# Performance work log

Measured on AMD Instinct MI355X. Metric: run time of the kernel, lower is better.

## Reference

```python
import jax, jax.numpy as jnp
import numpy as np

P, Q, R = 6, 0, 0
N = P + Q + R
DIM = 1 << N  # 64 basis blades


def _cayley_table(p, q, r):
    """Dense [dim, dim, dim] Cayley tensor C with C[a, b, a^b] = sign(a, b).
    Basis blades are indexed by bitmasks; sign combines the canonical
    reordering parity with the metric signature (+1 x p, -1 x q, 0 x r)."""
    n = p + q + r
    dim = 1 << n
    metric = [1.0] * p + [-1.0] * q + [0.0] * r
    C = np.zeros((dim, dim, dim), dtype=np.float32)
    for a in range(dim):
        for b in range(dim):
            # reorder parity: count transpositions to sort blade product
            s = 1.0
            aa = a >> 1
            cnt = 0
            while aa:
                cnt += bin(aa & b).count('1')
                aa >>= 1
            if cnt & 1:
                s = -s
            # metric contribution from repeated basis vectors
            for i in range(n):
                if (a >> i) & 1 and (b >> i) & 1:
                    s *= metric[i]
            C[a, b, a ^ b] = s
    return C

CAYLEY = jnp.asarray(_cayley_table(P, Q, R))  # [64, 64, 64], highly sparse


def setup_inputs() -> dict:
    key = jax.random.key(0)
    kx, kw = jax.random.split(key)
    x = jax.random.normal(kx, (1048576, DIM), dtype=jnp.float32)
    weight = jax.random.normal(kw, (DIM,), dtype=jnp.float32)
    return {"x": x, "weight": weight}


def reference(x, weight):
    # geometric_product(x, weight) with weight broadcast over the batch:
    # out[b, k] = sum_{i,j} C[i, j, k] * x[b, i] * weight[j]
    # Contract C with the shared weight first (tiny [dim, dim] matrix),
    # then apply to every batch element.
    M = jnp.einsum('ijk,j->ik', CAYLEY, weight)  # [64, 64]
    return x @ M  # [B, 64]
```

## Files before the change

kernel.cpp:

```cpp
#include <hip/hip_runtime.h>
#include <hip/hip_bf16.h>


#define DIM 64
#define TPB 256
#define ROWS 256

typedef __attribute__((ext_vector_type(8))) short  bf16x8;
typedef __attribute__((ext_vector_type(4))) float  f32x4;

__device__ __forceinline__ unsigned short f2bf(float v) {
    __hip_bfloat16 hb = __float2bfloat16(v);
    return *reinterpret_cast<unsigned short*>(&hb);
}

__global__ void build_Mt(const float* __restrict__ w, unsigned short* __restrict__ Mt) {
    int t = threadIdx.x + blockIdx.x * blockDim.x;
    if (t >= 8 * 64 * 8) return;
    int f  = t >> 9;
    int kc = f >> 2, ab = f & 3;
    int rem = t & 511;
    int l = rem >> 3, e = rem & 7;
    int k = kc * 32 + ((l >> 4) << 3) + e;
    int a = (ab << 4) + (l & 15);
    int j = k ^ a;
    int aa = k >> 1, cnt = 0;
    while (aa) { cnt += __popc(aa & j); aa >>= 1; }
    float v = (cnt & 1) ? -w[j] : w[j];
    Mt[t] = f2bf(v);
}

__global__ __launch_bounds__(TPB, 4)
void gp_main_kernel(const float* __restrict__ x,
                    const unsigned short* __restrict__ Mt,
                    float* __restrict__ out) {
    __shared__ unsigned short xs[ROWS * DIM];

    const int tid  = threadIdx.x;
    const int lane = tid & 63;
    const int wv   = tid >> 6;

    bf16x8 af[2][4];
    const bf16x8* __restrict__ Mtv = (const bf16x8*)Mt;
    #pragma unroll
    for (int kc = 0; kc < 2; ++kc)
        #pragma unroll
        for (int ab = 0; ab < 4; ++ab)
            af[kc][ab] = Mtv[(kc * 4 + ab) * 64 + lane];

    const long long rowbase = (long long)blockIdx.x * ROWS;
    const float4* __restrict__ xin = (const float4*)x + rowbase * 16;
    #pragma unroll
    for (int it = 0; it < 16; ++it) {
        int idx = it * TPB + tid;
        int row = idx >> 4;
        int c   = idx & 15;
        float4 v = xin[idx];
        int s    = c >> 1;
        int half = c & 1;
        unsigned short* dst = &xs[row * DIM + (((s ^ (row & 7)) << 3) | (half << 2))];
        ushort4 u = make_ushort4(f2bf(v.x), f2bf(v.y), f2bf(v.z), f2bf(v.w));
        *reinterpret_cast<ushort4*>(dst) = u;
    }
    __syncthreads();

    const int g = lane >> 4;
    float4* __restrict__ outp = (float4*)out;

    #pragma unroll
    for (int bb = 0; bb < 4; ++bb) {
        const int r_loc = wv * 64 + bb * 16 + (lane & 15);
        bf16x8 bfr[2];
        #pragma unroll
        for (int kc = 0; kc < 2; ++kc) {
            int s = kc * 4 + g;
            bfr[kc] = *reinterpret_cast<const bf16x8*>(
                &xs[r_loc * DIM + ((s ^ (r_loc & 7)) << 3)]);
        }
        f32x4 acc[4];
        #pragma unroll
        for (int ab = 0; ab < 4; ++ab) acc[ab] = (f32x4){0.f, 0.f, 0.f, 0.f};
        #pragma unroll
        for (int kc = 0; kc < 2; ++kc)
            #pragma unroll
            for (int ab = 0; ab < 4; ++ab)
                acc[ab] = __builtin_amdgcn_mfma_f32_16x16x32_bf16(
                    af[kc][ab], bfr[kc], acc[ab], 0, 0, 0);

        const long long rg = rowbase + r_loc;
        #pragma unroll
        for (int ab = 0; ab < 4; ++ab) {
            float4 o = make_float4(acc[ab][0], acc[ab][1], acc[ab][2], acc[ab][3]);
            outp[rg * 16 + ab * 4 + g] = o;
        }
    }
}

extern "C" void kernel_launch(void* const* d_in, const int* in_sizes, int n_in,
                              void* d_out, int out_size, void* d_ws, size_t ws_size,
                              hipStream_t stream) {
    const float* x = (const float*)d_in[0];
    const float* w = (const float*)d_in[1];
    float* out = (float*)d_out;
    unsigned short* Mt = (unsigned short*)d_ws;

    int nrows = in_sizes[0] / DIM;
    int nblocks = nrows / ROWS;

    build_Mt<<<16, 256, 0, stream>>>(w, Mt);
    gp_main_kernel<<<nblocks, TPB, 0, stream>>>(x, Mt, out);
}
```

Baseline: 111.3 us.

## Load x directly into MFMA operand registers, drop shared-memory staging

Removes the LDS staging buffer and block-wide barrier. Each wave now loads its own 64 rows of x straight from global memory into registers in the layout the MFMA B operand expects, then converts to bf16 in registers. This cuts LDS writes and reads, the sync, and 32KB of shared memory per block, which could raise occupancy. The cost is less coalesced global loads (each lane reads 32-byte chunks spread across rows) and higher register pressure from 16 float4s held per thread.

```diff
diff --git a/kernel.cpp b/kernel.cpp
--- a/kernel.cpp
+++ b/kernel.cpp
@@ -34,11 +34,11 @@
 void gp_main_kernel(const float* __restrict__ x,
                     const unsigned short* __restrict__ Mt,
                     float* __restrict__ out) {
-    __shared__ unsigned short xs[ROWS * DIM];
-
     const int tid  = threadIdx.x;
     const int lane = tid & 63;
     const int wv   = tid >> 6;
+    const int r15  = lane & 15;
+    const int g    = lane >> 4;
 
     bf16x8 af[2][4];
     const bf16x8* __restrict__ Mtv = (const bf16x8*)Mt;
@@ -48,35 +48,33 @@
         for (int ab = 0; ab < 4; ++ab)
             af[kc][ab] = Mtv[(kc * 4 + ab) * 64 + lane];
 
-    const long long rowbase = (long long)blockIdx.x * ROWS;
-    const float4* __restrict__ xin = (const float4*)x + rowbase * 16;
+    const long long rowbase = (long long)blockIdx.x * ROWS + (long long)wv * 64;
+
+    float4 raw[4][4];
     #pragma unroll
-    for (int it = 0; it < 16; ++it) {
-        int idx = it * TPB + tid;
-        int row = idx >> 4;
-        int c   = idx & 15;
-        float4 v = xin[idx];
-        int s    = c >> 1;
-        int half = c & 1;
-        unsigned short* dst = &xs[row * DIM + (((s ^ (row & 7)) << 3) | (half << 2))];
-        ushort4 u = make_ushort4(f2bf(v.x), f2bf(v.y), f2bf(v.z), f2bf(v.w));
-        *reinterpret_cast<ushort4*>(dst) = u;
+    for (int bb = 0; bb < 4; ++bb) {
+        const float4* __restrict__ p =
+            (const float4*)(x + (rowbase + bb * 16 + r15) * DIM) + g * 2;
+        raw[bb][0] = p[0];
+        raw[bb][1] = p[1];
+        raw[bb][2] = p[8];
+        raw[bb][3] = p[9];
     }
-    __syncthreads();
 
-    const int g = lane >> 4;
     float4* __restrict__ outp = (float4*)out;
 
     #pragma unroll
     for (int bb = 0; bb < 4; ++bb) {
-        const int r_loc = wv * 64 + bb * 16 + (lane & 15);
         bf16x8 bfr[2];
         #pragma unroll
         for (int kc = 0; kc < 2; ++kc) {
-            int s = kc * 4 + g;
-            bfr[kc] = *reinterpret_cast<const bf16x8*>(
-                &xs[r_loc * DIM + ((s ^ (r_loc & 7)) << 3)]);
+            const float* s = (const float*)&raw[bb][kc * 2];
+            bf16x8 t;
+            #pragma unroll
+            for (int e = 0; e < 8; ++e) t[e] = (short)f2bf(s[e]);
+            bfr[kc] = t;
         }
+
         f32x4 acc[4];
         #pragma unroll
         for (int ab = 0; ab < 4; ++ab) acc[ab] = (f32x4){0.f, 0.f, 0.f, 0.f};
@@ -87,12 +85,11 @@
                 acc[ab] = __builtin_amdgcn_mfma_f32_16x16x32_bf16(
                     af[kc][ab], bfr[kc], acc[ab], 0, 0, 0);
 
-        const long long rg = rowbase + r_loc;
+        const long long rg = rowbase + bb * 16 + r15;
         #pragma unroll
-        for (int ab = 0; ab < 4; ++ab) {
-            float4 o = make_float4(acc[ab][0], acc[ab][1], acc[ab][2], acc[ab][3]);
-            outp[rg * 16 + ab * 4 + g] = o;
-        }
+        for (int ab = 0; ab < 4; ++ab)
+            outp[rg * 16 + ab * 4 + g] =
+                make_float4(acc[ab][0], acc[ab][1], acc[ab][2], acc[ab][3]);
     }
 }
 
```

Result: slower. 123.1 us (+10.6%).
